# Kernel optimization log

Measured on AMD Instinct MI355X. Metric: run time of the kernel, lower is better.

The kernel has to match this reference:

```python
import jax, jax.numpy as jnp
import numpy as np

RADIUS = 3
DIAM = 2 * RADIUS + 1  # 7
NP = DIAM * DIAM       # 49 taps


def _cubic(d, a=-0.75):
    # torch bicubic kernel (a = -0.75)
    d = np.abs(d)
    return np.where(d <= 1, (a + 2) * d**3 - (a + 3) * d**2 + 1,
                    np.where(d < 2, a * d**3 - 5 * a * d**2 + 8 * a * d - 4 * a, 0.0))


def _resize_matrix(out_size, in_size):
    # dense [out,in] matrix reproducing torch F.interpolate bicubic, align_corners=False
    i = np.arange(out_size)
    x = (i + 0.5) * in_size / out_size - 0.5
    x0 = np.floor(x).astype(np.int64)
    t = x - x0
    W = np.zeros((out_size, in_size), np.float32)
    for k in range(-1, 3):
        w = _cubic(t - k)
        idx = np.clip(x0 + k, 0, in_size - 1)  # border replicate
        np.add.at(W, (i, idx), w.astype(np.float32))
    return jnp.asarray(W)


def _bicubic(x, GH, GW):
    B, C, H, W = x.shape
    Wh = _resize_matrix(GH, H)
    Ww = _resize_matrix(GW, W)
    return jnp.einsum('Hh,bchw,Ww->bcHW', Wh, x, Ww)


def _jbu(source, guidance, w1, b1, w2, b2, temp, sigma):
    # FeatUp JBULearnedRange.forward (eval mode: Dropout2d is identity)
    B, _, GH, GW = guidance.shape
    # range_proj: 1x1 conv -> GELU -> 1x1 conv
    q = jnp.einsum('kc,bchw->bkhw', w1, guidance) + b1[None, :, None, None]
    q = jax.nn.gelu(q, approximate=False)
    q = jnp.einsum('kc,bchw->bkhw', w2, q) + b2[None, :, None, None]  # [B,32,GH,GW]
    qp = jnp.pad(q, ((0, 0), (0, 0), (RADIUS, RADIUS), (RADIUS, RADIUS)), mode='reflect')
    # scores[b,p,h,w] = <key at center, key at offset p> (avoids B*32*49*H*W unfold)
    scores = jnp.stack([jnp.sum(qp[:, :, di:di + GH, dj:dj + GW] * q, axis=1)
                        for di in range(DIAM) for dj in range(DIAM)], axis=1)  # [B,49,GH,GW]
    t = jnp.clip(jnp.exp(temp), 1e-4, 1e4)
    range_kernel = jax.nn.softmax(t * scores, axis=1)
    dist = jnp.linspace(-1.0, 1.0, DIAM)
    gy, gx = jnp.meshgrid(dist, dist, indexing='ij')
    spatial_kernel = jnp.exp(-(gy**2 + gx**2) / (2.0 * sigma**2)).reshape(1, NP, 1, 1)
    k = range_kernel * spatial_kernel
    k = k / jnp.clip(jnp.sum(k, axis=1, keepdims=True), 1e-7, None)
    hr = _bicubic(source, GH, GW)
    hrp = jnp.pad(hr, ((0, 0), (0, 0), (RADIUS, RADIUS), (RADIUS, RADIUS)), mode='reflect')
    # AdaptiveConv: per-pixel 7x7 kernel applied to all channels
    out = jnp.zeros_like(hr)
    p_idx = 0
    for di in range(DIAM):
        for dj in range(DIAM):
            out = out + hrp[:, :, di:di + GH, dj:dj + GW] * k[:, p_idx][:, None]
            p_idx += 1
    return out


def _forward(x, guidance, linear_w, linear_b, w1s, b1s, w2s, b2s, temps, sigmas):
    f = (x @ linear_w.T + linear_b).reshape(-1, 3, 18, 18)
    for i in range(4):  # up1..up4, each fed the FULL guidance as in the Decoder
        f = _jbu(f, guidance, w1s[i], b1s[i], w2s[i], b2s[i], temps[i], sigmas[i])
    return f


def setup_inputs() -> dict:
    key = jax.random.key(0)
    ks = jax.random.split(key, 6)
    B = 8
    return {
        'x': jax.random.normal(ks[0], (B, 1000), jnp.float32),
        'guidance': jax.random.uniform(ks[1], (B, 3, 224, 224), jnp.float32),
        'linear_w': jax.random.normal(ks[2], (972, 1000), jnp.float32) * 0.03,
        'linear_b': jnp.zeros((972,), jnp.float32),
        'w1s': jax.random.normal(ks[3], (4, 32, 3), jnp.float32) * 0.1,
        'b1s': jnp.zeros((4, 32), jnp.float32),
        'w2s': jax.random.normal(ks[4], (4, 32, 32), jnp.float32) * 0.1,
        'b2s': jnp.zeros((4, 32), jnp.float32),
        'temps': jnp.zeros((4,), jnp.float32),   # range_temp init 0.0
        'sigmas': jnp.ones((4,), jnp.float32),   # sigma_spatial init 1.0
    }


def reference(x, guidance, linear_w, linear_b, w1s, b1s, w2s, b2s, temps, sigmas):
    return _forward(x, guidance, linear_w, linear_b, w1s, b1s, w2s, b2s, temps, sigmas)
```

## Files before the change

### kernel.cpp

```cpp
#include <hip/hip_runtime.h>
#include <hip/hip_fp16.h>
#include <math.h>

#define GHH 224
#define GWW 224
#define HW (GHH*GWW)
#define BATCH 8
#define RAD 3
#define DIAM 7
#define QC 32
#define TILE 16
#define TP (TILE + 2*RAD)
#define TPIX (TP*TP)
#define CS 485
#define SQ_B 31040

typedef _Float16 h2 __attribute__((ext_vector_type(2)));
typedef _Float16 v8h __attribute__((ext_vector_type(8)));
typedef float v4f __attribute__((ext_vector_type(4)));

#if defined(__has_builtin)
#if __has_builtin(__builtin_amdgcn_fdot2)
#define HAS_FDOT2 1
#endif
#endif

__device__ __forceinline__ h2 as_h2(float f) { union { float f; h2 h; } u; u.f = f; return u.h; }

__device__ __forceinline__ float dot2acc(float a, float b, float acc) {
#ifdef HAS_FDOT2
    return __builtin_amdgcn_fdot2(as_h2(a), as_h2(b), acc, false);
#else
    union { float f; __half2 h; } ua, ub; ua.f = a; ub.f = b;
    float2 fa = __half22float2(ua.h), fb = __half22float2(ub.h);
    return acc + fa.x * fb.x + fa.y * fb.y;
#endif
}

__device__ __forceinline__ float dot16(const float4& a, const float4& b, float acc) {
    acc = dot2acc(a.x, b.x, acc);
    acc = dot2acc(a.y, b.y, acc);
    acc = dot2acc(a.z, b.z, acc);
    acc = dot2acc(a.w, b.w, acc);
    return acc;
}

__device__ __forceinline__ int refl(int i) {
    if (i < 0) i = -i;
    if (i >= GHH) i = 2 * GHH - 2 - i;
    return i;
}

__device__ __forceinline__ float gelu_fast(float v) {
    float u = 0.7978845608f * v * (1.f + 0.044715f * v * v);
    float e = __expf(2.f * u);
    float th = 1.f - 2.f / (e + 1.f);
    return 0.5f * v * (1.f + th);
}

__global__ void linear_prep_kernel(const float* __restrict__ x,
                                   const float* __restrict__ W,
                                   const float* __restrict__ bias,
                                   float* __restrict__ f0,
                                   const float* __restrict__ w2s,
                                   __half* __restrict__ wsB,
                                   const float* __restrict__ w1s,
                                   const float* __restrict__ b1s,
                                   __half* __restrict__ wsW1,
                                   const float* __restrict__ guid,
                                   float4* __restrict__ guid4) {
    int blk = blockIdx.x;
    if (blk >= 1946) {
        int i = (blk - 1946) * 256 + threadIdx.x;
        int b = i / HW, pix = i % HW;
        guid4[i] = make_float4(guid[(b * 3) * HW + pix],
                               guid[(b * 3 + 1) * HW + pix],
                               guid[(b * 3 + 2) * HW + pix], 0.f);
        return;
    }
    if (blk == 1945) {
        int tid = threadIdx.x;
        if (tid < 128) {
            int s = tid >> 5, c = tid & 31;
            wsW1[tid * 4 + 0] = __float2half(w1s[s * 96 + c * 3 + 0]);
            wsW1[tid * 4 + 1] = __float2half(w1s[s * 96 + c * 3 + 1]);
            wsW1[tid * 4 + 2] = __float2half(w1s[s * 96 + c * 3 + 2]);
            wsW1[tid * 4 + 3] = __float2half(b1s[s * 32 + c]);
        }
        return;
    }
    if (blk == 1944) {
        int tid = threadIdx.x;
        int s = tid >> 6, l = tid & 63;
        int n0 = l & 15, kq = l >> 4;
        const float* w2 = w2s + s * 1024;
        __half* dst = wsB + (size_t)tid * 16;
        #pragma unroll
        for (int j = 0; j < 8; j++) {
            dst[j]     = __float2half(w2[n0 * QC + kq * 8 + j]);
            dst[8 + j] = __float2half(w2[(n0 + 16) * QC + kq * 8 + j]);
        }
        return;
    }
    int gwave = (blk * blockDim.x + threadIdx.x) >> 6;
    int lane = threadIdx.x & 63;
    if (gwave >= BATCH * 972) return;
    int b = gwave / 972, j = gwave % 972;
    const float* xr = x + b * 1000;
    const float* wr = W + j * 1000;
    float s = 0.f;
    for (int k = lane; k < 1000; k += 64)
        s += xr[k] * wr[k];
    #pragma unroll
    for (int off = 32; off; off >>= 1) s += __shfl_down(s, off, 64);
    if (lane == 0) f0[gwave] = s + bias[j];
}

__device__ __forceinline__ float cubicw(float d) {
    d = fabsf(d);
    if (d <= 1.f) return ((1.25f * d - 2.25f) * d) * d + 1.f;
    if (d < 2.f)  return ((-0.75f * d + 3.75f) * d - 6.f) * d + 3.f;
    return 0.f;
}

__global__ void bicubic_kernel(const float* __restrict__ f0, float4* __restrict__ hr4) {
    int idx = blockIdx.x * blockDim.x + threadIdx.x;
    if (idx >= BATCH * HW) return;
    int pix = idx % HW;
    int b = idx / HW;
    int w = pix % GWW, h = pix / GWW;
    float xx = (w + 0.5f) * (18.f / 224.f) - 0.5f;
    float yy = (h + 0.5f) * (18.f / 224.f) - 0.5f;
    float fx0 = floorf(xx), fy0 = floorf(yy);
    int x0 = (int)fx0, y0 = (int)fy0;
    float tx = xx - fx0, ty = yy - fy0;
    float wx[4], wy[4];
    int ix[4], iy[4];
    #pragma unroll
    for (int k = 0; k < 4; k++) {
        wx[k] = cubicw(tx - (float)(k - 1));
        wy[k] = cubicw(ty - (float)(k - 1));
        int a = x0 + (k - 1); ix[k] = min(max(a, 0), 17);
        a = y0 + (k - 1);     iy[k] = min(max(a, 0), 17);
    }
    float acc[3];
    #pragma unroll
    for (int c = 0; c < 3; c++) {
        const float* src = f0 + (b * 3 + c) * 324;
        float a = 0.f;
        #pragma unroll
        for (int ky = 0; ky < 4; ky++) {
            float rowv = 0.f;
            #pragma unroll
            for (int kx = 0; kx < 4; kx++) rowv += wx[kx] * src[iy[ky] * 18 + ix[kx]];
            a += wy[ky] * rowv;
        }
        acc[c] = a;
    }
    hr4[idx] = make_float4(acc[0], acc[1], acc[2], 0.f);
}

__global__ __launch_bounds__(256, 4) void jbu_kernel(
    const float4* __restrict__ guid4,
    const __half* __restrict__ wsW1,
    const __half* __restrict__ wsB, const float* __restrict__ b2,
    const float4* __restrict__ hr4,
    float4* __restrict__ out4,
    float* __restrict__ outP,
    const float* __restrict__ temps,
    const float* __restrict__ sigmas,
    int stage)
{
    __shared__ __align__(16) char smem[SQ_B + TPIX * 16];
    float4* sq = (float4*)smem;
    float4* sh = (float4*)(smem + SQ_B);

    const int tx = threadIdx.x, ty = threadIdx.y;
    const int tid = ty * TILE + tx;
    const int b = blockIdx.z;
    const int h0 = blockIdx.y * TILE, w0 = blockIdx.x * TILE;

    const bool interior = (h0 >= RAD) && (h0 + TILE + RAD <= GHH) &&
                          (w0 >= RAD) && (w0 + TILE + RAD <= GWW);
    if (interior) {
        const float4* hb = hr4 + (size_t)b * HW + (size_t)(h0 - RAD) * GWW + (w0 - RAD);
        for (int i = tid; i < TPIX; i += 256) {
            int r = i / TP, cx = i % TP;
            sh[i] = hb[(size_t)r * GWW + cx];
        }
    } else {
        for (int i = tid; i < TPIX; i += 256) {
            int r = i / TP, cx = i % TP;
            int gh = refl(h0 - RAD + r);
            int gw = refl(w0 - RAD + cx);
            sh[i] = hr4[(size_t)b * HW + (size_t)gh * GWW + gw];
        }
    }

    const int w = tid >> 6, l = tid & 63;
    const int n0 = l & 15, kq = l >> 4;
    const v8h* Bp = (const v8h*)(wsB + ((size_t)stage * 64 + l) * 16);
    const v8h W2a = Bp[0], W2b = Bp[1];
    const float4 b2a = *(const float4*)(b2 + 4 * kq);
    const float4 b2b = *(const float4*)(b2 + 16 + 4 * kq);
    union { _Float16 h[32]; float4 f4[4]; } W1;
    {
        const float4* wp = (const float4*)(wsW1 + stage * 128 + kq * 32);
        W1.f4[0] = wp[0]; W1.f4[1] = wp[1]; W1.f4[2] = wp[2]; W1.f4[3] = wp[3];
    }
    const int plane0 = kq >> 1;
    const int boff   = (kq & 1) * 8;

    #pragma unroll 1
    for (int r2 = 0; r2 < 2; r2++) {
        #pragma unroll
        for (int tt = 0; tt < 4; tt++) {
            int base = r2 * 256 + w * 64 + tt * 16;
            int p = base + n0;
            int pc = min(p, TPIX - 1);
            int rr = pc / TP, cc = pc - rr * TP;
            int gh = refl(h0 - RAD + rr), gw = refl(w0 - RAD + cc);
            float4 g = guid4[(size_t)b * HW + (size_t)gh * GWW + gw];
            union { _Float16 h[8]; v8h v; } A;
            #pragma unroll
            for (int j = 0; j < 8; j++) {
                float vv = fmaf((float)W1.h[j * 4], g.x,
                           fmaf((float)W1.h[j * 4 + 1], g.y,
                           fmaf((float)W1.h[j * 4 + 2], g.z, (float)W1.h[j * 4 + 3])));
                A.h[j] = (_Float16)gelu_fast(vv);
            }
            v4f D0 = {0.f, 0.f, 0.f, 0.f}, D1 = {0.f, 0.f, 0.f, 0.f};
            D0 = __builtin_amdgcn_mfma_f32_16x16x32_f16(W2a, A.v, D0, 0, 0, 0);
            D1 = __builtin_amdgcn_mfma_f32_16x16x32_f16(W2b, A.v, D1, 0, 0, 0);
            if (p < TPIX) {
                union { _Float16 h[4]; uint2 u; } q0, q1;
                q0.h[0] = (_Float16)(D0[0] + b2a.x);
                q0.h[1] = (_Float16)(D0[1] + b2a.y);
                q0.h[2] = (_Float16)(D0[2] + b2a.z);
                q0.h[3] = (_Float16)(D0[3] + b2a.w);
                q1.h[0] = (_Float16)(D1[0] + b2b.x);
                q1.h[1] = (_Float16)(D1[1] + b2b.y);
                q1.h[2] = (_Float16)(D1[2] + b2b.z);
                q1.h[3] = (_Float16)(D1[3] + b2b.w);
                *(uint2*)(smem + (plane0 * CS + p) * 16 + boff)       = q0.u;
                *(uint2*)(smem + ((2 + plane0) * CS + p) * 16 + boff) = q1.u;
            }
        }
    }
    __syncthreads();

    int ci = (ty + RAD) * TP + tx + RAD;
    float4 c0 = sq[ci], c1 = sq[CS + ci], c2 = sq[2 * CS + ci], c3 = sq[3 * CS + ci];

    float t = __expf(temps[stage]);
    t = fminf(fmaxf(t, 1e-4f), 1e4f);
    float sig = sigmas[stage];
    float inv2s2 = 1.f / (2.f * sig * sig);
    float sd[DIAM];
    #pragma unroll
    for (int i = 0; i < DIAM; i++) {
        float d = (float)(i - 3) * (1.f / 3.f);
        sd[i] = __expf(-d * d * inv2s2);
    }

    float es = 0.f, wsum = 0.f, o0 = 0.f, o1 = 0.f, o2 = 0.f;
    #pragma unroll
    for (int di = 0; di < DIAM; di++) {
        int rb = (ty + di) * TP + tx;
        float sy = sd[di];
        #pragma unroll
        for (int dj = 0; dj < DIAM; dj++) {
            int ni = rb + dj;
            float s = dot16(c0, sq[ni], 0.f);
            s = dot16(c1, sq[CS + ni], s);
            s = dot16(c2, sq[2 * CS + ni], s);
            s = dot16(c3, sq[3 * CS + ni], s);
            float4 hv = sh[ni];
            float e = __expf(t * s);
            float wgt = e * sy * sd[dj];
            es += e; wsum += wgt;
            o0 += wgt * hv.x; o1 += wgt * hv.y; o2 += wgt * hv.z;
        }
    }
    float rk = 1.f / fmaxf(wsum, 1e-7f * es);

    if (stage < 3) {
        out4[(size_t)b * HW + (size_t)(h0 + ty) * GWW + (w0 + tx)] =
            make_float4(o0 * rk, o1 * rk, o2 * rk, 0.f);
    } else {
        size_t obase = (size_t)b * 3 * HW + (size_t)(h0 + ty) * GWW + (w0 + tx);
        outP[obase]          = o0 * rk;
        outP[obase + HW]     = o1 * rk;
        outP[obase + 2 * HW] = o2 * rk;
    }
}

extern "C" void kernel_launch(void* const* d_in, const int* in_sizes, int n_in,
                              void* d_out, int out_size, void* d_ws, size_t ws_size,
                              hipStream_t stream) {
    const float* x      = (const float*)d_in[0];
    const float* guid   = (const float*)d_in[1];
    const float* lw     = (const float*)d_in[2];
    const float* lb     = (const float*)d_in[3];
    const float* w1s    = (const float*)d_in[4];
    const float* b1s    = (const float*)d_in[5];
    const float* w2s    = (const float*)d_in[6];
    const float* b2s    = (const float*)d_in[7];
    const float* temps  = (const float*)d_in[8];
    const float* sigmas = (const float*)d_in[9];

    char* ws = (char*)d_ws;
    const size_t P4_BYTES = (size_t)BATCH * HW * sizeof(float4);
    float4* guid4 = (float4*)ws;
    float4* hr4A  = (float4*)(ws + P4_BYTES);
    float4* hr4B  = (float4*)(ws + 2 * P4_BYTES);
    float*  f0    = (float*)(ws + 3 * P4_BYTES);
    __half* wsB   = (__half*)(ws + 3 * P4_BYTES + 31104);
    __half* wsW1  = (__half*)(ws + 3 * P4_BYTES + 31104 + 8192);

    linear_prep_kernel<<<1946 + 1568, 256, 0, stream>>>(
        x, lw, lb, f0, w2s, wsB, w1s, b1s, wsW1, guid, guid4);
    bicubic_kernel<<<(BATCH * HW + 255) / 256, 256, 0, stream>>>(f0, hr4A);

    dim3 jgrid(14, 14, BATCH), jblock(16, 16);
    const float4* hins[4]  = { hr4A, hr4B, hr4A, hr4B };
    float4*       fouts[4] = { hr4B, hr4A, hr4B, nullptr };
    for (int s = 0; s < 4; s++) {
        jbu_kernel<<<jgrid, jblock, 0, stream>>>(
            guid4, wsW1, wsB, b2s + s * 32,
            hins[s], fouts[s], (s == 3) ? (float*)d_out : nullptr,
            temps, sigmas, s);
    }
}
```

Measured before the change: 278.1 us.

## Compute two vertically adjacent output pixels per thread to reuse neighbor loads

Halves the block to 128 threads and makes each thread produce two output rows, so the 8 neighbor rows of shared-memory keys and hr values are loaded once and used for both pixels across the 6 overlapping rows. The range-projection MFMA loop is re-indexed for 2 waves doing 16 iterations. The intent is fewer LDS reads per output. In exchange, register pressure rises and each block has fewer waves to hide latency, with launch bounds changed to (128,2).

Measured after the change: 342.5 us. 1.23x slower.

```diff
diff --git a/kernel.cpp b/kernel.cpp
--- a/kernel.cpp
+++ b/kernel.cpp
@@ -160,7 +160,7 @@
     hr4[idx] = make_float4(acc[0], acc[1], acc[2], 0.f);
 }
 
-__global__ __launch_bounds__(256, 4) void jbu_kernel(
+__global__ __launch_bounds__(128, 2) void jbu_kernel(
     const float4* __restrict__ guid4,
     const __half* __restrict__ wsW1,
     const __half* __restrict__ wsB, const float* __restrict__ b2,
@@ -176,7 +176,7 @@
     float4* sh = (float4*)(smem + SQ_B);
 
     const int tx = threadIdx.x, ty = threadIdx.y;
-    const int tid = ty * TILE + tx;
+    const int tid = ty * 16 + tx;
     const int b = blockIdx.z;
     const int h0 = blockIdx.y * TILE, w0 = blockIdx.x * TILE;
 
@@ -184,12 +184,12 @@
                           (w0 >= RAD) && (w0 + TILE + RAD <= GWW);
     if (interior) {
         const float4* hb = hr4 + (size_t)b * HW + (size_t)(h0 - RAD) * GWW + (w0 - RAD);
-        for (int i = tid; i < TPIX; i += 256) {
+        for (int i = tid; i < TPIX; i += 128) {
             int r = i / TP, cx = i % TP;
             sh[i] = hb[(size_t)r * GWW + cx];
         }
     } else {
-        for (int i = tid; i < TPIX; i += 256) {
+        for (int i = tid; i < TPIX; i += 128) {
             int r = i / TP, cx = i % TP;
             int gh = refl(h0 - RAD + r);
             int gw = refl(w0 - RAD + cx);
@@ -211,46 +211,43 @@
     const int plane0 = kq >> 1;
     const int boff   = (kq & 1) * 8;
 
-    #pragma unroll 1
-    for (int r2 = 0; r2 < 2; r2++) {
-        #pragma unroll
-        for (int tt = 0; tt < 4; tt++) {
-            int base = r2 * 256 + w * 64 + tt * 16;
-            int p = base + n0;
-            int pc = min(p, TPIX - 1);
-            int rr = pc / TP, cc = pc - rr * TP;
-            int gh = refl(h0 - RAD + rr), gw = refl(w0 - RAD + cc);
-            float4 g = guid4[(size_t)b * HW + (size_t)gh * GWW + gw];
-            union { _Float16 h[8]; v8h v; } A;
-            #pragma unroll
-            for (int j = 0; j < 8; j++) {
-                float vv = fmaf((float)W1.h[j * 4], g.x,
-                           fmaf((float)W1.h[j * 4 + 1], g.y,
-                           fmaf((float)W1.h[j * 4 + 2], g.z, (float)W1.h[j * 4 + 3])));
-                A.h[j] = (_Float16)gelu_fast(vv);
-            }
-            v4f D0 = {0.f, 0.f, 0.f, 0.f}, D1 = {0.f, 0.f, 0.f, 0.f};
-            D0 = __builtin_amdgcn_mfma_f32_16x16x32_f16(W2a, A.v, D0, 0, 0, 0);
-            D1 = __builtin_amdgcn_mfma_f32_16x16x32_f16(W2b, A.v, D1, 0, 0, 0);
-            if (p < TPIX) {
-                union { _Float16 h[4]; uint2 u; } q0, q1;
-                q0.h[0] = (_Float16)(D0[0] + b2a.x);
-                q0.h[1] = (_Float16)(D0[1] + b2a.y);
-                q0.h[2] = (_Float16)(D0[2] + b2a.z);
-                q0.h[3] = (_Float16)(D0[3] + b2a.w);
-                q1.h[0] = (_Float16)(D1[0] + b2b.x);
-                q1.h[1] = (_Float16)(D1[1] + b2b.y);
-                q1.h[2] = (_Float16)(D1[2] + b2b.z);
-                q1.h[3] = (_Float16)(D1[3] + b2b.w);
-                *(uint2*)(smem + (plane0 * CS + p) * 16 + boff)       = q0.u;
-                *(uint2*)(smem + ((2 + plane0) * CS + p) * 16 + boff) = q1.u;
-            }
+    #pragma unroll 4
+    for (int it = 0; it < 16; it++) {
+        int p = it * 32 + w * 16 + n0;
+        int pc = min(p, TPIX - 1);
+        int rr = pc / TP, cc = pc - rr * TP;
+        int gh = refl(h0 - RAD + rr), gw = refl(w0 - RAD + cc);
+        float4 g = guid4[(size_t)b * HW + (size_t)gh * GWW + gw];
+        union { _Float16 h[8]; v8h v; } A;
+        #pragma unroll
+        for (int j = 0; j < 8; j++) {
+            float vv = fmaf((float)W1.h[j * 4], g.x,
+                       fmaf((float)W1.h[j * 4 + 1], g.y,
+                       fmaf((float)W1.h[j * 4 + 2], g.z, (float)W1.h[j * 4 + 3])));
+            A.h[j] = (_Float16)gelu_fast(vv);
+        }
+        v4f D0 = {0.f, 0.f, 0.f, 0.f}, D1 = {0.f, 0.f, 0.f, 0.f};
+        D0 = __builtin_amdgcn_mfma_f32_16x16x32_f16(W2a, A.v, D0, 0, 0, 0);
+        D1 = __builtin_amdgcn_mfma_f32_16x16x32_f16(W2b, A.v, D1, 0, 0, 0);
+        if (p < TPIX) {
+            union { _Float16 h[4]; uint2 u; } q0, q1;
+            q0.h[0] = (_Float16)(D0[0] + b2a.x);
+            q0.h[1] = (_Float16)(D0[1] + b2a.y);
+            q0.h[2] = (_Float16)(D0[2] + b2a.z);
+            q0.h[3] = (_Float16)(D0[3] + b2a.w);
+            q1.h[0] = (_Float16)(D1[0] + b2b.x);
+            q1.h[1] = (_Float16)(D1[1] + b2b.y);
+            q1.h[2] = (_Float16)(D1[2] + b2b.z);
+            q1.h[3] = (_Float16)(D1[3] + b2b.w);
+            *(uint2*)(smem + (plane0 * CS + p) * 16 + boff)       = q0.u;
+            *(uint2*)(smem + ((2 + plane0) * CS + p) * 16 + boff) = q1.u;
         }
     }
     __syncthreads();
 
-    int ci = (ty + RAD) * TP + tx + RAD;
-    float4 c0 = sq[ci], c1 = sq[CS + ci], c2 = sq[2 * CS + ci], c3 = sq[3 * CS + ci];
+    const int ci = (2 * ty + RAD) * TP + tx + RAD;
+    float4 c00 = sq[ci],      c01 = sq[CS + ci],      c02 = sq[2*CS + ci],      c03 = sq[3*CS + ci];
+    float4 c10 = sq[ci + TP], c11 = sq[CS + ci + TP], c12 = sq[2*CS + ci + TP], c13 = sq[3*CS + ci + TP];
 
     float t = __expf(temps[stage]);
     t = fminf(fmaxf(t, 1e-4f), 1e4f);
@@ -263,35 +260,86 @@
         sd[i] = __expf(-d * d * inv2s2);
     }
 
-    float es = 0.f, wsum = 0.f, o0 = 0.f, o1 = 0.f, o2 = 0.f;
-    #pragma unroll
-    for (int di = 0; di < DIAM; di++) {
-        int rb = (ty + di) * TP + tx;
-        float sy = sd[di];
+    float es0 = 0.f, ws0 = 0.f, o00 = 0.f, o01 = 0.f, o02 = 0.f;
+    float es1 = 0.f, ws1 = 0.f, o10 = 0.f, o11 = 0.f, o12 = 0.f;
+
+    {
+        const int rb = (2 * ty) * TP + tx;
+        const float sy = sd[0];
         #pragma unroll
         for (int dj = 0; dj < DIAM; dj++) {
             int ni = rb + dj;
-            float s = dot16(c0, sq[ni], 0.f);
-            s = dot16(c1, sq[CS + ni], s);
-            s = dot16(c2, sq[2 * CS + ni], s);
-            s = dot16(c3, sq[3 * CS + ni], s);
+            float4 q0 = sq[ni], q1 = sq[CS + ni], q2 = sq[2*CS + ni], q3 = sq[3*CS + ni];
             float4 hv = sh[ni];
-            float e = __expf(t * s);
-            float wgt = e * sy * sd[dj];
-            es += e; wsum += wgt;
-            o0 += wgt * hv.x; o1 += wgt * hv.y; o2 += wgt * hv.z;
-        }
-    }
-    float rk = 1.f / fmaxf(wsum, 1e-7f * es);
-
+            float sa = dot16(c00, q0, 0.f); sa = dot16(c01, q1, sa);
+            float sb = dot16(c02, q2, 0.f); sb = dot16(c03, q3, sb);
+            float e = __expf(t * (sa + sb));
+            float wg = e * (sy * sd[dj]);
+            es0 += e; ws0 += wg;
+            o00 += wg * hv.x; o01 += wg * hv.y; o02 += wg * hv.z;
+        }
+    }
+    float syp = sd[0];
+    #pragma unroll 1
+    for (int rr = 1; rr < DIAM; rr++) {
+        const int rb = (2 * ty + rr) * TP + tx;
+        float dd = (float)(rr - 3) * (1.f / 3.f);
+        float sy = __expf(-dd * dd * inv2s2);
+        #pragma unroll
+        for (int dj = 0; dj < DIAM; dj++) {
+            int ni = rb + dj;
+            float4 q0 = sq[ni], q1 = sq[CS + ni], q2 = sq[2*CS + ni], q3 = sq[3*CS + ni];
+            float4 hv = sh[ni];
+            float sa0 = dot16(c00, q0, 0.f); sa0 = dot16(c01, q1, sa0);
+            float sb0 = dot16(c02, q2, 0.f); sb0 = dot16(c03, q3, sb0);
+            float sa1 = dot16(c10, q0, 0.f); sa1 = dot16(c11, q1, sa1);
+            float sb1 = dot16(c12, q2, 0.f); sb1 = dot16(c13, q3, sb1);
+            float e0 = __expf(t * (sa0 + sb0));
+            float e1 = __expf(t * (sa1 + sb1));
+            float sdj = sd[dj];
+            float wg0 = e0 * (sy * sdj);
+            float wg1 = e1 * (syp * sdj);
+            es0 += e0; ws0 += wg0;
+            o00 += wg0 * hv.x; o01 += wg0 * hv.y; o02 += wg0 * hv.z;
+            es1 += e1; ws1 += wg1;
+            o10 += wg1 * hv.x; o11 += wg1 * hv.y; o12 += wg1 * hv.z;
+        }
+        syp = sy;
+    }
+    {
+        const int rb = (2 * ty + 7) * TP + tx;
+        const float sy = syp;
+        #pragma unroll
+        for (int dj = 0; dj < DIAM; dj++) {
+            int ni = rb + dj;
+            float4 q0 = sq[ni], q1 = sq[CS + ni], q2 = sq[2*CS + ni], q3 = sq[3*CS + ni];
+            float4 hv = sh[ni];
+            float sa = dot16(c10, q0, 0.f); sa = dot16(c11, q1, sa);
+            float sb = dot16(c12, q2, 0.f); sb = dot16(c13, q3, sb);
+            float e = __expf(t * (sa + sb));
+            float wg = e * (sy * sd[dj]);
+            es1 += e; ws1 += wg;
+            o10 += wg * hv.x; o11 += wg * hv.y; o12 += wg * hv.z;
+        }
+    }
+
+    float rk0 = 1.f / fmaxf(ws0, 1e-7f * es0);
+    float rk1 = 1.f / fmaxf(ws1, 1e-7f * es1);
+    const int y0 = h0 + 2 * ty;
     if (stage < 3) {
-        out4[(size_t)b * HW + (size_t)(h0 + ty) * GWW + (w0 + tx)] =
-            make_float4(o0 * rk, o1 * rk, o2 * rk, 0.f);
+        out4[(size_t)b * HW + (size_t)y0 * GWW + (w0 + tx)] =
+            make_float4(o00 * rk0, o01 * rk0, o02 * rk0, 0.f);
+        out4[(size_t)b * HW + (size_t)(y0 + 1) * GWW + (w0 + tx)] =
+            make_float4(o10 * rk1, o11 * rk1, o12 * rk1, 0.f);
     } else {
-        size_t obase = (size_t)b * 3 * HW + (size_t)(h0 + ty) * GWW + (w0 + tx);
-        outP[obase]          = o0 * rk;
-        outP[obase + HW]     = o1 * rk;
-        outP[obase + 2 * HW] = o2 * rk;
+        size_t ob0 = (size_t)b * 3 * HW + (size_t)y0 * GWW + (w0 + tx);
+        outP[ob0]          = o00 * rk0;
+        outP[ob0 + HW]     = o01 * rk0;
+        outP[ob0 + 2 * HW] = o02 * rk0;
+        size_t ob1 = ob0 + GWW;
+        outP[ob1]          = o10 * rk1;
+        outP[ob1 + HW]     = o11 * rk1;
+        outP[ob1 + 2 * HW] = o12 * rk1;
     }
 }
 
@@ -322,7 +370,7 @@
         x, lw, lb, f0, w2s, wsB, w1s, b1s, wsW1, guid, guid4);
     bicubic_kernel<<<(BATCH * HW + 255) / 256, 256, 0, stream>>>(f0, hr4A);
 
-    dim3 jgrid(14, 14, BATCH), jblock(16, 16);
+    dim3 jgrid(14, 14, BATCH), jblock(16, 8);
     const float4* hins[4]  = { hr4A, hr4B, hr4A, hr4B };
     float4*       fouts[4] = { hr4B, hr4A, hr4B, nullptr };
     for (int s = 0; s < 4; s++) {
```

## Compute JBU scores and weighted aggregation with MFMA instead of scalar dot products

Applied to the files above, without the earlier changes.

Replaces the per-thread scalar fdot2 score loop and the scalar weighted sum with MFMA 16x16x32 f16 matrix ops. Each wave handles a tile row: one MFMA computes scores for neighbour columns and another aggregates values. Values are stored in shared memory as split hi/lo f16 planes plus a ones plane, so the normaliser comes out of the same MFMA. It also drops the interior fast path for staging the tile and the es-based clamp in the denominator. The gains are higher matrix-unit throughput; the costs are extra MFMA work on redundant padded columns, f16 weights, and a change to the normalisation clamp.

Result: slower. 287.3 us (+3.3%).

```diff
diff --git a/kernel.cpp b/kernel.cpp
--- a/kernel.cpp
+++ b/kernel.cpp
@@ -13,37 +13,15 @@
 #define TP (TILE + 2*RAD)
 #define TPIX (TP*TP)
 #define CS 485
-#define SQ_B 31040
+
+#define HRH_COLS 24
+#define PSTR (TP*HRH_COLS)
+#define HRH_B (8*PSTR*2)
+#define SMEM_B (HRH_B + 4*CS*16)
 
 typedef _Float16 h2 __attribute__((ext_vector_type(2)));
 typedef _Float16 v8h __attribute__((ext_vector_type(8)));
 typedef float v4f __attribute__((ext_vector_type(4)));
-
-#if defined(__has_builtin)
-#if __has_builtin(__builtin_amdgcn_fdot2)
-#define HAS_FDOT2 1
-#endif
-#endif
-
-__device__ __forceinline__ h2 as_h2(float f) { union { float f; h2 h; } u; u.f = f; return u.h; }
-
-__device__ __forceinline__ float dot2acc(float a, float b, float acc) {
-#ifdef HAS_FDOT2
-    return __builtin_amdgcn_fdot2(as_h2(a), as_h2(b), acc, false);
-#else
-    union { float f; __half2 h; } ua, ub; ua.f = a; ub.f = b;
-    float2 fa = __half22float2(ua.h), fb = __half22float2(ub.h);
-    return acc + fa.x * fb.x + fa.y * fb.y;
-#endif
-}
-
-__device__ __forceinline__ float dot16(const float4& a, const float4& b, float acc) {
-    acc = dot2acc(a.x, b.x, acc);
-    acc = dot2acc(a.y, b.y, acc);
-    acc = dot2acc(a.z, b.z, acc);
-    acc = dot2acc(a.w, b.w, acc);
-    return acc;
-}
 
 __device__ __forceinline__ int refl(int i) {
     if (i < 0) i = -i;
@@ -171,30 +149,34 @@
     const float* __restrict__ sigmas,
     int stage)
 {
-    __shared__ __align__(16) char smem[SQ_B + TPIX * 16];
-    float4* sq = (float4*)smem;
-    float4* sh = (float4*)(smem + SQ_B);
+    __shared__ __align__(16) char smem[SMEM_B];
+    _Float16* hrh = (_Float16*)smem;
+    char* sqb = smem + HRH_B;
 
     const int tx = threadIdx.x, ty = threadIdx.y;
     const int tid = ty * TILE + tx;
     const int b = blockIdx.z;
     const int h0 = blockIdx.y * TILE, w0 = blockIdx.x * TILE;
 
-    const bool interior = (h0 >= RAD) && (h0 + TILE + RAD <= GHH) &&
-                          (w0 >= RAD) && (w0 + TILE + RAD <= GWW);
-    if (interior) {
-        const float4* hb = hr4 + (size_t)b * HW + (size_t)(h0 - RAD) * GWW + (w0 - RAD);
-        for (int i = tid; i < TPIX; i += 256) {
-            int r = i / TP, cx = i % TP;
-            sh[i] = hb[(size_t)r * GWW + cx];
-        }
-    } else {
-        for (int i = tid; i < TPIX; i += 256) {
-            int r = i / TP, cx = i % TP;
-            int gh = refl(h0 - RAD + r);
-            int gw = refl(w0 - RAD + cx);
-            sh[i] = hr4[(size_t)b * HW + (size_t)gh * GWW + gw];
-        }
+    for (int i = tid; i < TPIX; i += 256) {
+        int r = i / TP, cx = i % TP;
+        int gh = refl(h0 - RAD + r), gw = refl(w0 - RAD + cx);
+        float4 v = hr4[(size_t)b * HW + (size_t)gh * GWW + gw];
+        _Float16 hx = (_Float16)v.x, hy = (_Float16)v.y, hz = (_Float16)v.z;
+        int base = r * HRH_COLS + cx;
+        hrh[0 * PSTR + base] = hx;
+        hrh[1 * PSTR + base] = hy;
+        hrh[2 * PSTR + base] = hz;
+        hrh[3 * PSTR + base] = (_Float16)1.0f;
+        hrh[4 * PSTR + base] = (_Float16)(v.x - (float)hx);
+        hrh[5 * PSTR + base] = (_Float16)(v.y - (float)hy);
+        hrh[6 * PSTR + base] = (_Float16)(v.z - (float)hz);
+        hrh[7 * PSTR + base] = (_Float16)0.0f;
+    }
+    for (int i = tid; i < 8 * TP * 2; i += 256) {
+        int p = i / (TP * 2), rem = i % (TP * 2);
+        int r = rem >> 1, cc = 22 + (rem & 1);
+        hrh[p * PSTR + r * HRH_COLS + cc] = (_Float16)0.0f;
     }
 
     const int w = tid >> 6, l = tid & 63;
@@ -242,56 +224,75 @@
                 q1.h[1] = (_Float16)(D1[1] + b2b.y);
                 q1.h[2] = (_Float16)(D1[2] + b2b.z);
                 q1.h[3] = (_Float16)(D1[3] + b2b.w);
-                *(uint2*)(smem + (plane0 * CS + p) * 16 + boff)       = q0.u;
-                *(uint2*)(smem + ((2 + plane0) * CS + p) * 16 + boff) = q1.u;
+                *(uint2*)(sqb + (plane0 * CS + p) * 16 + boff)       = q0.u;
+                *(uint2*)(sqb + ((2 + plane0) * CS + p) * 16 + boff) = q1.u;
             }
         }
     }
     __syncthreads();
 
-    int ci = (ty + RAD) * TP + tx + RAD;
-    float4 c0 = sq[ci], c1 = sq[CS + ci], c2 = sq[2 * CS + ci], c3 = sq[3 * CS + ci];
+    const int wv = tid >> 6;
+    const int g = l >> 4, c = l & 15;
 
     float t = __expf(temps[stage]);
     t = fminf(fmaxf(t, 1e-4f), 1e4f);
     float sig = sigmas[stage];
     float inv2s2 = 1.f / (2.f * sig * sig);
-    float sd[DIAM];
+    float sdv[DIAM];
     #pragma unroll
     for (int i = 0; i < DIAM; i++) {
         float d = (float)(i - 3) * (1.f / 3.f);
-        sd[i] = __expf(-d * d * inv2s2);
-    }
-
-    float es = 0.f, wsum = 0.f, o0 = 0.f, o1 = 0.f, o2 = 0.f;
-    #pragma unroll
-    for (int di = 0; di < DIAM; di++) {
-        int rb = (ty + di) * TP + tx;
-        float sy = sd[di];
+        sdv[i] = __expf(-d * d * inv2s2);
+    }
+    float lc[8];
+    #pragma unroll
+    for (int jj = 0; jj < 8; jj++) {
+        int dj = 8 * g + jj - c;
+        float d = (float)(dj - 3) * (1.f / 3.f);
+        lc[jj] = (dj >= 0 && dj <= 6) ? (-d * d * inv2s2) : -1e38f;
+    }
+    const int nbb = 8 * (c >> 2) + (c & 3);
+    const int nb0 = min(nbb, 21);
+    const int nb1 = min(nbb + 4, 21);
+    const int pA = c & 3;
+
+    #pragma unroll 1
+    for (int rr = 0; rr < 4; rr++) {
+        const int row = wv * 4 + rr;
+        const v8h Bc = *(const v8h*)(sqb + (size_t)(g * CS + (row + RAD) * TP + RAD + c) * 16);
+        v4f D2 = {0.f, 0.f, 0.f, 0.f};
         #pragma unroll
-        for (int dj = 0; dj < DIAM; dj++) {
-            int ni = rb + dj;
-            float s = dot16(c0, sq[ni], 0.f);
-            s = dot16(c1, sq[CS + ni], s);
-            s = dot16(c2, sq[2 * CS + ni], s);
-            s = dot16(c3, sq[3 * CS + ni], s);
-            float4 hv = sh[ni];
-            float e = __expf(t * s);
-            float wgt = e * sy * sd[dj];
-            es += e; wsum += wgt;
-            o0 += wgt * hv.x; o1 += wgt * hv.y; o2 += wgt * hv.z;
-        }
-    }
-    float rk = 1.f / fmaxf(wsum, 1e-7f * es);
-
-    if (stage < 3) {
-        out4[(size_t)b * HW + (size_t)(h0 + ty) * GWW + (w0 + tx)] =
-            make_float4(o0 * rk, o1 * rk, o2 * rk, 0.f);
-    } else {
-        size_t obase = (size_t)b * 3 * HW + (size_t)(h0 + ty) * GWW + (w0 + tx);
-        outP[obase]          = o0 * rk;
-        outP[obase + HW]     = o1 * rk;
-        outP[obase + 2 * HW] = o2 * rk;
+        for (int di = 0; di < DIAM; di++) {
+            const int prow = row + di;
+            const v8h A0 = *(const v8h*)(sqb + (size_t)(g * CS + prow * TP + nb0) * 16);
+            const v8h A1 = *(const v8h*)(sqb + (size_t)(g * CS + prow * TP + nb1) * 16);
+            v4f S0 = {0.f, 0.f, 0.f, 0.f}, S1 = {0.f, 0.f, 0.f, 0.f};
+            S0 = __builtin_amdgcn_mfma_f32_16x16x32_f16(A0, Bc, S0, 0, 0, 0);
+            S1 = __builtin_amdgcn_mfma_f32_16x16x32_f16(A1, Bc, S1, 0, 0, 0);
+            const float sy = sdv[di];
+            union { _Float16 h[8]; v8h v; } Wg;
+            #pragma unroll
+            for (int j = 0; j < 4; j++) {
+                Wg.h[j]     = (_Float16)(__expf(fmaf(S0[j], t, lc[j])) * sy);
+                Wg.h[4 + j] = (_Float16)(__expf(fmaf(S1[j], t, lc[4 + j])) * sy);
+            }
+            const v8h Hh = *(const v8h*)(smem + (size_t)((pA * TP + prow) * HRH_COLS + 8 * g) * 2);
+            const v8h Hl = *(const v8h*)(smem + (size_t)(((pA + 4) * TP + prow) * HRH_COLS + 8 * g) * 2);
+            D2 = __builtin_amdgcn_mfma_f32_16x16x32_f16(Hh, Wg.v, D2, 0, 0, 0);
+            D2 = __builtin_amdgcn_mfma_f32_16x16x32_f16(Hl, Wg.v, D2, 0, 0, 0);
+        }
+        if (l < 16) {
+            float rk = 1.f / fmaxf(D2[3], 1e-7f);
+            if (stage < 3) {
+                out4[(size_t)b * HW + (size_t)(h0 + row) * GWW + (w0 + c)] =
+                    make_float4(D2[0] * rk, D2[1] * rk, D2[2] * rk, 0.f);
+            } else {
+                size_t obase = (size_t)b * 3 * HW + (size_t)(h0 + row) * GWW + (w0 + c);
+                outP[obase]          = D2[0] * rk;
+                outP[obase + HW]     = D2[1] * rk;
+                outP[obase + 2 * HW] = D2[2] * rk;
+            }
+        }
     }
 }
 
```
